# Kernel optimization log

Measured on AMD Instinct MI355X. Metric: run time of the kernel, lower is better.

## Reference

```python
import jax, jax.numpy as jnp
import numpy as np

B, N, C, H = 8, 1024, 1024, 16
HD = C // H
SCALE = HD ** -0.5

def setup_inputs() -> dict:
    key = jax.random.key(0)
    k1, k2, k3, k4 = jax.random.split(key, 4)
    x = jax.random.normal(k1, (B, N, C), dtype=jnp.float32)
    # torch nn.Linear weights: [out, in]
    w_qkv = jax.random.normal(k2, (3 * C, C), dtype=jnp.float32) * (C ** -0.5)
    w_proj = jax.random.normal(k3, (C, C), dtype=jnp.float32) * (C ** -0.5)
    b_proj = jax.random.normal(k4, (C,), dtype=jnp.float32) * 0.02
    return {"x": x, "w_qkv": w_qkv, "w_proj": w_proj, "b_proj": b_proj}

def reference(x, w_qkv, w_proj, b_proj):
    Bv, Nv, Cv = x.shape
    # qkv projection (no bias); torch Linear: x @ W^T
    qkv = jnp.einsum('bnc,dc->bnd', x, w_qkv)
    qkv = qkv.reshape(Bv, Nv, 3, H, HD).transpose(2, 0, 3, 1, 4)  # [3,B,H,N,hd]
    q, k, v = qkv[0], qkv[1], qkv[2]
    attn = jnp.einsum('bhnd,bhmd->bhnm', q, k) * SCALE  # [B,H,N,N]
    attn = jax.nn.softmax(attn, axis=-1)
    out = jnp.einsum('bhnm,bhmd->bhnd', attn, v)
    out = out.transpose(0, 2, 1, 3).reshape(Bv, Nv, Cv)
    out = jnp.einsum('bnc,dc->bnd', out, w_proj) + b_proj
    return out
```

## Files before the change

### kernel.cpp

```cpp
#include <hip/hip_runtime.h>


typedef __attribute__((ext_vector_type(8))) short bf16x8;
typedef __attribute__((ext_vector_type(4))) short bf16x4;
typedef __attribute__((ext_vector_type(4))) float f32x4;

__device__ __forceinline__ short f2bf(float f) {
    union { float f; unsigned u; } x;
    x.f = f;
    unsigned r = x.u + 0x7fffu + ((x.u >> 16) & 1u);
    return (short)(r >> 16);
}

__device__ __forceinline__ void load_lds16(const void* g, void* l) {
    __builtin_amdgcn_global_load_lds((const __attribute__((address_space(1))) unsigned*)g,
                                     (__attribute__((address_space(3))) unsigned*)l,
                                     16, 0, 0);
}

__global__ __launch_bounds__(256) void convert_all(const float* __restrict__ x,
                                                   const float* __restrict__ wqkv,
                                                   const float* __restrict__ wproj,
                                                   short* __restrict__ xb,
                                                   short* __restrict__ wqkvb,
                                                   short* __restrict__ wprojb) {
    int i = blockIdx.x * 256 + threadIdx.x;
    const float* src;
    short* dst;
    int j;
    if (i < 2097152)      { src = x;     dst = xb;     j = i; }
    else if (i < 2883584) { src = wqkv;  dst = wqkvb;  j = i - 2097152; }
    else                  { src = wproj; dst = wprojb; j = i - 2883584; }
    float4 v = *(const float4*)(src + j * 4);
    unsigned lo = (unsigned short)f2bf(v.x) | ((unsigned)(unsigned short)f2bf(v.y) << 16);
    unsigned hi = (unsigned short)f2bf(v.z) | ((unsigned)(unsigned short)f2bf(v.w) << 16);
    uint2 p; p.x = lo; p.y = hi;
    *(uint2*)(dst + j * 4) = p;
}

template<int EPI, int NTX>
__global__ __launch_bounds__(256, 3) void gemm97(const short* __restrict__ A,
                                                 const short* __restrict__ Bt,
                                                 short* __restrict__ q,
                                                 short* __restrict__ kk,
                                                 short* __restrict__ vt,
                                                 const float* __restrict__ bias,
                                                 float* __restrict__ out) {
    __shared__ alignas(16) short As[128][64];
    __shared__ alignas(16) short Bs[128][64];
    const int K = 1024;
    constexpr int NWG = 64 * NTX;
    constexpr int CHUNK = NWG / 8;

    const int bid = blockIdx.x;
    const int tile = (bid & 7) * CHUNK + (bid >> 3);
    const int m0 = (tile / NTX) * 128;
    const int n0 = (tile % NTX) * 128;

    const int t = threadIdx.x;
    const int w = t >> 6, lane = t & 63, quad = lane >> 4, l16 = lane & 15;
    const int wm = (w >> 1) * 64, wn = (w & 1) * 64;
    const int sw = l16 & 7;

    const int srow = t >> 3;
    const int scol = ((t & 7) ^ (srow & 7)) * 8;
    const short* Ag = A  + (m0 + srow) * K + scol;
    const short* Bg = Bt + (n0 + srow) * K + scol;
    short* const Asw = &As[w * 8][0];
    short* const Bsw = &Bs[w * 8][0];

    f32x4 acc[4][4];
    #pragma unroll
    for (int mi = 0; mi < 4; ++mi)
        #pragma unroll
        for (int ni = 0; ni < 4; ++ni) acc[mi][ni] = (f32x4){0.f, 0.f, 0.f, 0.f};

    #pragma unroll 1
    for (int kt = 0; kt < 16; ++kt) {
        __syncthreads();
        #pragma unroll
        for (int r = 0; r < 4; ++r)
            load_lds16(Ag + r * 32 * K + kt * 64, Asw + r * 32 * 64);
        #pragma unroll
        for (int r = 0; r < 4; ++r)
            load_lds16(Bg + r * 32 * K + kt * 64, Bsw + r * 32 * 64);
        __syncthreads();

        bf16x8 af[4][2], bf[4][2];
        #pragma unroll
        for (int mi = 0; mi < 4; ++mi)
            #pragma unroll
            for (int c = 0; c < 2; ++c)
                af[mi][c] = *(const bf16x8*)&As[wm + mi * 16 + l16][((quad + 4 * c) ^ sw) * 8];
        #pragma unroll
        for (int ni = 0; ni < 4; ++ni)
            #pragma unroll
            for (int c = 0; c < 2; ++c)
                bf[ni][c] = *(const bf16x8*)&Bs[wn + ni * 16 + l16][((quad + 4 * c) ^ sw) * 8];
        #pragma unroll
        for (int mi = 0; mi < 4; ++mi)
            #pragma unroll
            for (int ni = 0; ni < 4; ++ni) {
                acc[mi][ni] = __builtin_amdgcn_mfma_f32_16x16x32_bf16(af[mi][0], bf[ni][0], acc[mi][ni], 0, 0, 0);
                acc[mi][ni] = __builtin_amdgcn_mfma_f32_16x16x32_bf16(af[mi][1], bf[ni][1], acc[mi][ni], 0, 0, 0);
            }
    }

    if (EPI == 0) {
        const float QS = 0.125f * 1.44269504088896f;
        #pragma unroll
        for (int ni = 0; ni < 4; ++ni) {
            int col = n0 + wn + ni * 16 + l16;
            int sect = col >> 10;
            int c = col & 1023;
            int h = c >> 6, dd = c & 63;
            #pragma unroll
            for (int mi = 0; mi < 4; ++mi) {
                #pragma unroll
                for (int r = 0; r < 4; ++r) {
                    int m = m0 + wm + mi * 16 + quad * 4 + r;
                    int b = m >> 10, i = m & 1023;
                    float v = acc[mi][ni][r];
                    if (sect == 0)      q[((b * 16 + h) * 1024 + i) * 64 + dd] = f2bf(v * QS);
                    else if (sect == 1) kk[((b * 16 + h) * 1024 + i) * 64 + dd] = f2bf(v);
                    else                vt[((b * 16 + h) * 64 + dd) * 1024 + i] = f2bf(v);
                }
            }
        }
    } else {
        #pragma unroll
        for (int ni = 0; ni < 4; ++ni) {
            int col = n0 + wn + ni * 16 + l16;
            float bv = bias[col];
            #pragma unroll
            for (int mi = 0; mi < 4; ++mi) {
                #pragma unroll
                for (int r = 0; r < 4; ++r) {
                    int m = m0 + wm + mi * 16 + quad * 4 + r;
                    out[m * 1024 + col] = acc[mi][ni][r] + bv;
                }
            }
        }
    }
}

__global__ __launch_bounds__(256) void attn_kernel(const short* __restrict__ q,
                                                   const short* __restrict__ k,
                                                   const short* __restrict__ vt,
                                                   short* __restrict__ ao) {
    __shared__ alignas(16) short Ks[2][64][72];
    __shared__ alignas(16) short Vs[2][64][72];

    const int bh = blockIdx.y, qt = blockIdx.x;
    const int t = threadIdx.x, w = t >> 6, lane = t & 63, quad = lane >> 4, l16 = lane & 15;
    const short* qg = q  + (bh * 1024 + qt * 128) * 64;
    const short* kg = k  + bh * 65536;
    const short* vg = vt + bh * 65536;

    bf16x8 qf[2][2];
    for (int mi = 0; mi < 2; ++mi) {
        const short* qr = qg + (w * 32 + mi * 16 + l16) * 64;
        qf[mi][0] = *(const bf16x8*)(qr + quad * 8);
        qf[mi][1] = *(const bf16x8*)(qr + 32 + quad * 8);
    }

    const int r0 = t >> 3,          c80 = (t & 7) * 8;
    const int r1 = (t + 256) >> 3,  c81 = c80;

    float rs[2] = {0.f, 0.f};
    f32x4 oaccT[2][4];
    for (int mi = 0; mi < 2; ++mi)
        for (int dt = 0; dt < 4; ++dt) oaccT[mi][dt] = (f32x4){0.f, 0.f, 0.f, 0.f};

    {
        float4 a = *(const float4*)&kg[r0 * 64 + c80];
        float4 b = *(const float4*)&kg[r1 * 64 + c81];
        float4 c = *(const float4*)&vg[r0 * 1024 + c80];
        float4 d = *(const float4*)&vg[r1 * 1024 + c81];
        *(float4*)&Ks[0][r0][c80] = a;  *(float4*)&Ks[0][r1][c81] = b;
        *(float4*)&Vs[0][r0][c80] = c;  *(float4*)&Vs[0][r1][c81] = d;
    }

    for (int jt = 0; jt < 16; ++jt) {
        const int cur = jt & 1;
        asm volatile("s_waitcnt lgkmcnt(0)" ::: "memory");
        asm volatile("s_barrier" ::: "memory");

        float4 kr0, kr1, vr0, vr1;
        if (jt < 15) {
            int jn = jt + 1;
            kr0 = *(const float4*)&kg[(jn * 64 + r0) * 64 + c80];
            kr1 = *(const float4*)&kg[(jn * 64 + r1) * 64 + c81];
            vr0 = *(const float4*)&vg[r0 * 1024 + jn * 64 + c80];
            vr1 = *(const float4*)&vg[r1 * 1024 + jn * 64 + c81];
        }

        for (int js = 0; js < 4; ++js) {
            bf16x8 kf0 = *(const bf16x8*)&Ks[cur][js * 16 + l16][quad * 8];
            bf16x8 kf1 = *(const bf16x8*)&Ks[cur][js * 16 + l16][32 + quad * 8];
            bf16x4 vtf[4];
            for (int dt = 0; dt < 4; ++dt)
                vtf[dt] = *(const bf16x4*)&Vs[cur][dt * 16 + l16][js * 16 + quad * 4];
            for (int mi = 0; mi < 2; ++mi) {
                f32x4 s = (f32x4){0.f, 0.f, 0.f, 0.f};
                s = __builtin_amdgcn_mfma_f32_16x16x32_bf16(kf0, qf[mi][0], s, 0, 0, 0);
                s = __builtin_amdgcn_mfma_f32_16x16x32_bf16(kf1, qf[mi][1], s, 0, 0, 0);
                bf16x4 pfrag;
                for (int r = 0; r < 4; ++r) {
                    float p = __builtin_amdgcn_exp2f(s[r]);
                    rs[mi] += p;
                    pfrag[r] = f2bf(p);
                }
                for (int dt = 0; dt < 4; ++dt)
                    oaccT[mi][dt] = __builtin_amdgcn_mfma_f32_16x16x16bf16_1k(
                        vtf[dt], pfrag, oaccT[mi][dt], 0, 0, 0);
            }
        }

        if (jt < 15) {
            const int nxt = cur ^ 1;
            *(float4*)&Ks[nxt][r0][c80] = kr0;  *(float4*)&Ks[nxt][r1][c81] = kr1;
            *(float4*)&Vs[nxt][r0][c80] = vr0;  *(float4*)&Vs[nxt][r1][c81] = vr1;
        }
    }

    for (int mi = 0; mi < 2; ++mi) {
        rs[mi] += __shfl_xor(rs[mi], 16, 64);
        rs[mi] += __shfl_xor(rs[mi], 32, 64);
    }

    const int b = bh >> 4, h = bh & 15;
    for (int mi = 0; mi < 2; ++mi) {
        float inv = 1.0f / rs[mi];
        int i = qt * 128 + w * 32 + mi * 16 + l16;
        short* aor = ao + (b * 1024 + i) * 1024 + h * 64;
        for (int dt = 0; dt < 4; ++dt) {
            bf16x4 o4;
            for (int r = 0; r < 4; ++r) o4[r] = f2bf(oaccT[mi][dt][r] * inv);
            *(bf16x4*)(aor + dt * 16 + quad * 4) = o4;
        }
    }
}

extern "C" void kernel_launch(void* const* d_in, const int* in_sizes, int n_in,
                              void* d_out, int out_size, void* d_ws, size_t ws_size,
                              hipStream_t stream) {
    const float* x      = (const float*)d_in[0];
    const float* w_qkv  = (const float*)d_in[1];
    const float* w_proj = (const float*)d_in[2];
    const float* b_proj = (const float*)d_in[3];
    float* out = (float*)d_out;

    char* ws = (char*)d_ws;
    short* xb     = (short*)(ws);
    short* wqkvb  = (short*)(ws + 16777216);
    short* wprojb = (short*)(ws + 23068672);
    short* qb     = (short*)(ws + 25165824);
    short* kb     = (short*)(ws + 41943040);
    short* vtb    = (short*)(ws + 58720256);
    short* aob    = (short*)(ws + 75497472);

    convert_all<<<12288, 256, 0, stream>>>(x, w_qkv, w_proj, xb, wqkvb, wprojb);
    gemm97<0, 24><<<1536, 256, 0, stream>>>(xb, wqkvb, qb, kb, vtb, nullptr, nullptr);
    attn_kernel<<<dim3(8, 128), 256, 0, stream>>>(qb, kb, vtb, aob);
    gemm97<1, 8><<<512, 256, 0, stream>>>(aob, wprojb, nullptr, nullptr, nullptr, b_proj, out);
}
```

Measured before the change: 240.0 us.

## Rewrite GEMMs with 256x256 tiles, 8 waves, and double-buffered async LDS staging

Replaces the 128x128 single-buffered GEMM with a 256x256 tile kernel using 512 threads and 128KB of dynamic LDS. The next K-tile is prefetched into the other buffer while the current one is consumed, with vmcnt and barrier waits placed by hand and s_setprio raised around MFMA bursts. The goal is to hide global-load latency and improve data reuse per loaded byte. The cost is fewer workgroups: 384 and 128 blocks on a GPU with 256 CUs, which may cause wave-quantization losses, especially in the projection GEMM. It also brings higher register pressure and hand-tuned waitcnt counts that are easy to get wrong.

```diff
diff --git a/kernel.cpp b/kernel.cpp
--- a/kernel.cpp
+++ b/kernel.cpp
@@ -39,72 +39,120 @@
 }
 
 template<int EPI, int NTX>
-__global__ __launch_bounds__(256, 3) void gemm97(const short* __restrict__ A,
+__global__ __launch_bounds__(512, 2) void gemmkp(const short* __restrict__ A,
                                                  const short* __restrict__ Bt,
                                                  short* __restrict__ q,
                                                  short* __restrict__ kk,
                                                  short* __restrict__ vt,
                                                  const float* __restrict__ bias,
                                                  float* __restrict__ out) {
-    __shared__ alignas(16) short As[128][64];
-    __shared__ alignas(16) short Bs[128][64];
+    extern __shared__ short lds[];
+    short* const As = lds;
+    short* const Bs = lds + 32768;
     const int K = 1024;
-    constexpr int NWG = 64 * NTX;
+    constexpr int NWG = 32 * NTX;
     constexpr int CHUNK = NWG / 8;
 
     const int bid = blockIdx.x;
     const int tile = (bid & 7) * CHUNK + (bid >> 3);
-    const int m0 = (tile / NTX) * 128;
-    const int n0 = (tile % NTX) * 128;
+    const int m0 = (tile / NTX) * 256;
+    const int n0 = (tile % NTX) * 256;
 
     const int t = threadIdx.x;
     const int w = t >> 6, lane = t & 63, quad = lane >> 4, l16 = lane & 15;
-    const int wm = (w >> 1) * 64, wn = (w & 1) * 64;
-    const int sw = l16 & 7;
-
-    const int srow = t >> 3;
-    const int scol = ((t & 7) ^ (srow & 7)) * 8;
-    const short* Ag = A  + (m0 + srow) * K + scol;
-    const short* Bg = Bt + (n0 + srow) * K + scol;
-    short* const Asw = &As[w * 8][0];
-    short* const Bsw = &Bs[w * 8][0];
-
-    f32x4 acc[4][4];
+    const int wm = (w >> 2) * 128, wn = (w & 3) * 64;
+    const int swA = l16 & 7, swB = (l16 >> 1) & 3;
+
+    const int srA = t >> 3;
+    const int scA = ((t & 7) ^ (srA & 7)) * 8;
+    const int srB = t >> 2;
+    const int scB = ((t & 3) ^ ((srB >> 1) & 3)) * 8;
+
+    const short* Ag = A  + (m0 + srA) * K + scA;
+    const short* Bg = Bt + (n0 + srB) * K + scB;
+
+    f32x4 acc[8][4];
     #pragma unroll
-    for (int mi = 0; mi < 4; ++mi)
+    for (int mi = 0; mi < 8; ++mi)
         #pragma unroll
         for (int ni = 0; ni < 4; ++ni) acc[mi][ni] = (f32x4){0.f, 0.f, 0.f, 0.f};
 
+    bf16x8 af[4], bf[4];
+
+#define STG_A(kt_, h_) do { \
+    load_lds16(Ag + ((h_) * 64) * 1024 + (kt_) * 64, \
+               As + ((kt_) & 1) * 16384 + ((h_) * 64 + w * 8) * 64); \
+    load_lds16(Ag + ((h_) * 64 + 128) * 1024 + (kt_) * 64, \
+               As + ((kt_) & 1) * 16384 + ((h_) * 64 + 128 + w * 8) * 64); } while (0)
+#define STG_B(kt_, kap_) do { \
+    load_lds16(Bg + (kt_) * 64 + (kap_) * 32, \
+               Bs + ((kt_) & 1) * 16384 + (kap_) * 8192 + (w * 16) * 32); \
+    load_lds16(Bg + 128 * 1024 + (kt_) * 64 + (kap_) * 32, \
+               Bs + ((kt_) & 1) * 16384 + (kap_) * 8192 + (128 + w * 16) * 32); } while (0)
+
+#define READ_FRAGS(h_, kap_) do { \
+    _Pragma("unroll") \
+    for (int mi = 0; mi < 4; ++mi) \
+        af[mi] = *(const bf16x8*)(Ar + (wm + (h_) * 64 + mi * 16 + l16) * 64 + (((kap_) * 4 + quad) ^ swA) * 8); \
+    _Pragma("unroll") \
+    for (int ni = 0; ni < 4; ++ni) \
+        bf[ni] = *(const bf16x8*)(Br + (kap_) * 8192 + (wn + ni * 16 + l16) * 32 + (quad ^ swB) * 8); } while (0)
+
+#define MFMA16(h_) do { \
+    __builtin_amdgcn_s_setprio(1); \
+    _Pragma("unroll") \
+    for (int mi = 0; mi < 4; ++mi) \
+        _Pragma("unroll") \
+        for (int ni = 0; ni < 4; ++ni) \
+            acc[(h_) * 4 + mi][ni] = __builtin_amdgcn_mfma_f32_16x16x32_bf16(af[mi], bf[ni], acc[(h_) * 4 + mi][ni], 0, 0, 0); \
+    __builtin_amdgcn_s_setprio(0); } while (0)
+
+#define BAR   asm volatile("s_barrier" ::: "memory")
+#define LGKM0 asm volatile("s_waitcnt lgkmcnt(0)" ::: "memory")
+#define VM(n) asm volatile("s_waitcnt vmcnt(" #n ")" ::: "memory")
+
+    STG_A(0, 0); STG_B(0, 0); STG_A(0, 1); STG_B(0, 1);
+    STG_A(1, 0); STG_B(1, 0);
+    VM(8);
+    BAR;
+
     #pragma unroll 1
     for (int kt = 0; kt < 16; ++kt) {
-        __syncthreads();
-        #pragma unroll
-        for (int r = 0; r < 4; ++r)
-            load_lds16(Ag + r * 32 * K + kt * 64, Asw + r * 32 * 64);
-        #pragma unroll
-        for (int r = 0; r < 4; ++r)
-            load_lds16(Bg + r * 32 * K + kt * 64, Bsw + r * 32 * 64);
-        __syncthreads();
-
-        bf16x8 af[4][2], bf[4][2];
-        #pragma unroll
-        for (int mi = 0; mi < 4; ++mi)
-            #pragma unroll
-            for (int c = 0; c < 2; ++c)
-                af[mi][c] = *(const bf16x8*)&As[wm + mi * 16 + l16][((quad + 4 * c) ^ sw) * 8];
-        #pragma unroll
-        for (int ni = 0; ni < 4; ++ni)
-            #pragma unroll
-            for (int c = 0; c < 2; ++c)
-                bf[ni][c] = *(const bf16x8*)&Bs[wn + ni * 16 + l16][((quad + 4 * c) ^ sw) * 8];
-        #pragma unroll
-        for (int mi = 0; mi < 4; ++mi)
-            #pragma unroll
-            for (int ni = 0; ni < 4; ++ni) {
-                acc[mi][ni] = __builtin_amdgcn_mfma_f32_16x16x32_bf16(af[mi][0], bf[ni][0], acc[mi][ni], 0, 0, 0);
-                acc[mi][ni] = __builtin_amdgcn_mfma_f32_16x16x32_bf16(af[mi][1], bf[ni][1], acc[mi][ni], 0, 0, 0);
-            }
-    }
+        const short* Ar = As + (kt & 1) * 16384;
+        const short* Br = Bs + (kt & 1) * 16384;
+
+        READ_FRAGS(0, 0);
+        if (kt < 15) { STG_A(kt + 1, 1); STG_B(kt + 1, 1); }
+        BAR; LGKM0;
+        MFMA16(0);
+        if (kt < 15) VM(8); else VM(0);
+        BAR;
+
+        READ_FRAGS(0, 1);
+        BAR; LGKM0;
+        MFMA16(0);
+        BAR;
+
+        READ_FRAGS(1, 0);
+        if (kt < 14) STG_A(kt + 2, 0);
+        BAR; LGKM0;
+        MFMA16(1);
+        BAR;
+
+        READ_FRAGS(1, 1);
+        if (kt < 14) STG_B(kt + 2, 0);
+        BAR; LGKM0;
+        MFMA16(1);
+        if (kt < 14) VM(8); else if (kt == 14) VM(4);
+        BAR;
+    }
+#undef STG_A
+#undef STG_B
+#undef READ_FRAGS
+#undef MFMA16
+#undef BAR
+#undef LGKM0
+#undef VM
 
     if (EPI == 0) {
         const float QS = 0.125f * 1.44269504088896f;
@@ -115,7 +163,7 @@
             int c = col & 1023;
             int h = c >> 6, dd = c & 63;
             #pragma unroll
-            for (int mi = 0; mi < 4; ++mi) {
+            for (int mi = 0; mi < 8; ++mi) {
                 #pragma unroll
                 for (int r = 0; r < 4; ++r) {
                     int m = m0 + wm + mi * 16 + quad * 4 + r;
@@ -133,7 +181,7 @@
             int col = n0 + wn + ni * 16 + l16;
             float bv = bias[col];
             #pragma unroll
-            for (int mi = 0; mi < 4; ++mi) {
+            for (int mi = 0; mi < 8; ++mi) {
                 #pragma unroll
                 for (int r = 0; r < 4; ++r) {
                     int m = m0 + wm + mi * 16 + quad * 4 + r;
@@ -260,8 +308,17 @@
     short* vtb    = (short*)(ws + 58720256);
     short* aob    = (short*)(ws + 75497472);
 
+    static bool s_init = false;
+    if (!s_init) {
+        hipFuncSetAttribute(reinterpret_cast<const void*>(&gemmkp<0, 12>),
+                            hipFuncAttributeMaxDynamicSharedMemorySize, 131072);
+        hipFuncSetAttribute(reinterpret_cast<const void*>(&gemmkp<1, 4>),
+                            hipFuncAttributeMaxDynamicSharedMemorySize, 131072);
+        s_init = true;
+    }
+
     convert_all<<<12288, 256, 0, stream>>>(x, w_qkv, w_proj, xb, wqkvb, wprojb);
-    gemm97<0, 24><<<1536, 256, 0, stream>>>(xb, wqkvb, qb, kb, vtb, nullptr, nullptr);
+    gemmkp<0, 12><<<384, 512, 131072, stream>>>(xb, wqkvb, qb, kb, vtb, nullptr, nullptr);
     attn_kernel<<<dim3(8, 128), 256, 0, stream>>>(qb, kb, vtb, aob);
-    gemm97<1, 8><<<512, 256, 0, stream>>>(aob, wprojb, nullptr, nullptr, nullptr, b_proj, out);
-}
+    gemmkp<1, 4><<<128, 512, 131072, stream>>>(aob, wprojb, nullptr, nullptr, nullptr, b_proj, out);
+}
```

New measurement: 280.7 us. 17.0% more time.

## Double-buffer LDS tiles in GEMM kernels to overlap global loads with MFMA

Applied to the files above, without the earlier changes.

Converts both GEMM kernels to a two-stage LDS pipeline using 64KB of dynamic shared memory, prefetching the next K tile while the current one feeds the MFMAs. This removes one of the two barriers per iteration and is meant to hide global-to-LDS load latency. In exchange, LDS use doubles and the launch bound drops from 3 to 2 workgroups per CU, which lowers occupancy.

```diff
diff --git a/kernel.cpp b/kernel.cpp
--- a/kernel.cpp
+++ b/kernel.cpp
@@ -39,15 +39,14 @@
 }
 
 template<int EPI, int NTX>
-__global__ __launch_bounds__(256, 3) void gemm97(const short* __restrict__ A,
+__global__ __launch_bounds__(256, 2) void gemmdb(const short* __restrict__ A,
                                                  const short* __restrict__ Bt,
                                                  short* __restrict__ q,
                                                  short* __restrict__ kk,
                                                  short* __restrict__ vt,
                                                  const float* __restrict__ bias,
                                                  float* __restrict__ out) {
-    __shared__ alignas(16) short As[128][64];
-    __shared__ alignas(16) short Bs[128][64];
+    extern __shared__ short lds[];
     const int K = 1024;
     constexpr int NWG = 64 * NTX;
     constexpr int CHUNK = NWG / 8;
@@ -66,8 +65,7 @@
     const int scol = ((t & 7) ^ (srow & 7)) * 8;
     const short* Ag = A  + (m0 + srow) * K + scol;
     const short* Bg = Bt + (n0 + srow) * K + scol;
-    short* const Asw = &As[w * 8][0];
-    short* const Bsw = &Bs[w * 8][0];
+    const int w8 = w * 8 * 64;
 
     f32x4 acc[4][4];
     #pragma unroll
@@ -75,28 +73,35 @@
         #pragma unroll
         for (int ni = 0; ni < 4; ++ni) acc[mi][ni] = (f32x4){0.f, 0.f, 0.f, 0.f};
 
+#define STG(kt_, d_) do { \
+    _Pragma("unroll") \
+    for (int r = 0; r < 4; ++r) \
+        load_lds16(Ag + r * 32 * K + (kt_) * 64, lds + (d_) * 8192 + r * 32 * 64 + w8); \
+    _Pragma("unroll") \
+    for (int r = 0; r < 4; ++r) \
+        load_lds16(Bg + r * 32 * K + (kt_) * 64, lds + 16384 + (d_) * 8192 + r * 32 * 64 + w8); } while (0)
+
+    STG(0, 0);
+    __syncthreads();
+
     #pragma unroll 1
     for (int kt = 0; kt < 16; ++kt) {
-        __syncthreads();
-        #pragma unroll
-        for (int r = 0; r < 4; ++r)
-            load_lds16(Ag + r * 32 * K + kt * 64, Asw + r * 32 * 64);
-        #pragma unroll
-        for (int r = 0; r < 4; ++r)
-            load_lds16(Bg + r * 32 * K + kt * 64, Bsw + r * 32 * 64);
-        __syncthreads();
-
+        const int d = kt & 1;
+        if (kt < 15) STG(kt + 1, d ^ 1);
+
+        const short* Ar = lds + d * 8192;
+        const short* Br = lds + 16384 + d * 8192;
         bf16x8 af[4][2], bf[4][2];
         #pragma unroll
         for (int mi = 0; mi < 4; ++mi)
             #pragma unroll
             for (int c = 0; c < 2; ++c)
-                af[mi][c] = *(const bf16x8*)&As[wm + mi * 16 + l16][((quad + 4 * c) ^ sw) * 8];
+                af[mi][c] = *(const bf16x8*)(Ar + (wm + mi * 16 + l16) * 64 + (((quad + 4 * c) ^ sw) * 8));
         #pragma unroll
         for (int ni = 0; ni < 4; ++ni)
             #pragma unroll
             for (int c = 0; c < 2; ++c)
-                bf[ni][c] = *(const bf16x8*)&Bs[wn + ni * 16 + l16][((quad + 4 * c) ^ sw) * 8];
+                bf[ni][c] = *(const bf16x8*)(Br + (wn + ni * 16 + l16) * 64 + (((quad + 4 * c) ^ sw) * 8));
         #pragma unroll
         for (int mi = 0; mi < 4; ++mi)
             #pragma unroll
@@ -104,7 +109,9 @@
                 acc[mi][ni] = __builtin_amdgcn_mfma_f32_16x16x32_bf16(af[mi][0], bf[ni][0], acc[mi][ni], 0, 0, 0);
                 acc[mi][ni] = __builtin_amdgcn_mfma_f32_16x16x32_bf16(af[mi][1], bf[ni][1], acc[mi][ni], 0, 0, 0);
             }
-    }
+        if (kt < 15) __syncthreads();
+    }
+#undef STG
 
     if (EPI == 0) {
         const float QS = 0.125f * 1.44269504088896f;
@@ -260,8 +267,17 @@
     short* vtb    = (short*)(ws + 58720256);
     short* aob    = (short*)(ws + 75497472);
 
+    static bool s_init = false;
+    if (!s_init) {
+        hipFuncSetAttribute(reinterpret_cast<const void*>(&gemmdb<0, 24>),
+                            hipFuncAttributeMaxDynamicSharedMemorySize, 65536);
+        hipFuncSetAttribute(reinterpret_cast<const void*>(&gemmdb<1, 8>),
+                            hipFuncAttributeMaxDynamicSharedMemorySize, 65536);
+        s_init = true;
+    }
+
     convert_all<<<12288, 256, 0, stream>>>(x, w_qkv, w_proj, xb, wqkvb, wprojb);
-    gemm97<0, 24><<<1536, 256, 0, stream>>>(xb, wqkvb, qb, kb, vtb, nullptr, nullptr);
+    gemmdb<0, 24><<<1536, 256, 65536, stream>>>(xb, wqkvb, qb, kb, vtb, nullptr, nullptr);
     attn_kernel<<<dim3(8, 128), 256, 0, stream>>>(qb, kb, vtb, aob);
-    gemm97<1, 8><<<512, 256, 0, stream>>>(aob, wprojb, nullptr, nullptr, nullptr, b_proj, out);
-}
+    gemmdb<1, 8><<<512, 256, 65536, stream>>>(aob, wprojb, nullptr, nullptr, nullptr, b_proj, out);
+}
```

New measurement: 254.2 us. +5.9%, slower.

## Double-buffer QKV GEMM in dynamic LDS with 8 waves per block

Applied to the files above, without the earlier changes.

Splits the templated GEMM into a dedicated QKV kernel and a projection kernel. The QKV kernel now uses 512 threads (8 waves, each computing a 64x32 sub-tile) and double-buffered LDS staging through global_load_lds, so the next K-tile loads while the current one is multiplied. That takes one barrier per iteration and is meant to hide global memory latency. In exchange it uses 64KB of dynamic LDS, which can limit occupancy, and each wave does less MFMA work per LDS fragment read.

```diff
diff --git a/kernel.cpp b/kernel.cpp
--- a/kernel.cpp
+++ b/kernel.cpp
@@ -38,17 +38,109 @@
     *(uint2*)(dst + j * 4) = p;
 }
 
-template<int EPI, int NTX>
-__global__ __launch_bounds__(256, 3) void gemm97(const short* __restrict__ A,
-                                                 const short* __restrict__ Bt,
-                                                 short* __restrict__ q,
-                                                 short* __restrict__ kk,
-                                                 short* __restrict__ vt,
-                                                 const float* __restrict__ bias,
-                                                 float* __restrict__ out) {
+__global__ __launch_bounds__(512, 4) void gemm_qkv5(const short* __restrict__ A,
+                                                    const short* __restrict__ Bt,
+                                                    short* __restrict__ q,
+                                                    short* __restrict__ kk,
+                                                    short* __restrict__ vt) {
+    extern __shared__ short lds[];
+    const int K = 1024;
+    constexpr int NTX = 24;
+    constexpr int NWG = 64 * NTX;
+    constexpr int CHUNK = NWG / 8;
+
+    const int bid = blockIdx.x;
+    const int tile = (bid & 7) * CHUNK + (bid >> 3);
+    const int m0 = (tile / NTX) * 128;
+    const int n0 = (tile % NTX) * 128;
+
+    const int t = threadIdx.x;
+    const int w = t >> 6, lane = t & 63, quad = lane >> 4, l16 = lane & 15;
+    const int wm = (w >> 2) * 64, wn = (w & 3) * 32;
+    const int sw = l16 & 7;
+
+    const int srow = t >> 3;
+    const int scol = ((t & 7) ^ (srow & 7)) * 8;
+    const short* Ag = A  + (m0 + srow) * K + scol;
+    const short* Bg = Bt + (n0 + srow) * K + scol;
+    const int w8 = w * 8 * 64;
+
+    f32x4 acc[4][2];
+    #pragma unroll
+    for (int mi = 0; mi < 4; ++mi)
+        #pragma unroll
+        for (int ni = 0; ni < 2; ++ni) acc[mi][ni] = (f32x4){0.f, 0.f, 0.f, 0.f};
+
+#define STG(kt_, d_) do { \
+    _Pragma("unroll") \
+    for (int r = 0; r < 2; ++r) \
+        load_lds16(Ag + r * 64 * K + (kt_) * 64, lds + (d_) * 8192 + r * 64 * 64 + w8); \
+    _Pragma("unroll") \
+    for (int r = 0; r < 2; ++r) \
+        load_lds16(Bg + r * 64 * K + (kt_) * 64, lds + 16384 + (d_) * 8192 + r * 64 * 64 + w8); } while (0)
+
+    STG(0, 0);
+    __syncthreads();
+
+    #pragma unroll 1
+    for (int kt = 0; kt < 16; ++kt) {
+        const int d = kt & 1;
+        if (kt < 15) STG(kt + 1, d ^ 1);
+
+        const short* Ar = lds + d * 8192;
+        const short* Br = lds + 16384 + d * 8192;
+        bf16x8 af[4][2], bf[2][2];
+        #pragma unroll
+        for (int mi = 0; mi < 4; ++mi)
+            #pragma unroll
+            for (int c = 0; c < 2; ++c)
+                af[mi][c] = *(const bf16x8*)(Ar + (wm + mi * 16 + l16) * 64 + (((quad + 4 * c) ^ sw) * 8));
+        #pragma unroll
+        for (int ni = 0; ni < 2; ++ni)
+            #pragma unroll
+            for (int c = 0; c < 2; ++c)
+                bf[ni][c] = *(const bf16x8*)(Br + (wn + ni * 16 + l16) * 64 + (((quad + 4 * c) ^ sw) * 8));
+        #pragma unroll
+        for (int mi = 0; mi < 4; ++mi)
+            #pragma unroll
+            for (int ni = 0; ni < 2; ++ni) {
+                acc[mi][ni] = __builtin_amdgcn_mfma_f32_16x16x32_bf16(af[mi][0], bf[ni][0], acc[mi][ni], 0, 0, 0);
+                acc[mi][ni] = __builtin_amdgcn_mfma_f32_16x16x32_bf16(af[mi][1], bf[ni][1], acc[mi][ni], 0, 0, 0);
+            }
+        if (kt < 15) __syncthreads();
+    }
+#undef STG
+
+    const float QS = 0.125f * 1.44269504088896f;
+    #pragma unroll
+    for (int ni = 0; ni < 2; ++ni) {
+        int col = n0 + wn + ni * 16 + l16;
+        int sect = col >> 10;
+        int c = col & 1023;
+        int h = c >> 6, dd = c & 63;
+        #pragma unroll
+        for (int mi = 0; mi < 4; ++mi) {
+            #pragma unroll
+            for (int r = 0; r < 4; ++r) {
+                int m = m0 + wm + mi * 16 + quad * 4 + r;
+                int b = m >> 10, i = m & 1023;
+                float v = acc[mi][ni][r];
+                if (sect == 0)      q[((b * 16 + h) * 1024 + i) * 64 + dd] = f2bf(v * QS);
+                else if (sect == 1) kk[((b * 16 + h) * 1024 + i) * 64 + dd] = f2bf(v);
+                else                vt[((b * 16 + h) * 64 + dd) * 1024 + i] = f2bf(v);
+            }
+        }
+    }
+}
+
+__global__ __launch_bounds__(256, 3) void gemm_proj9(const short* __restrict__ A,
+                                                     const short* __restrict__ Bt,
+                                                     const float* __restrict__ bias,
+                                                     float* __restrict__ out) {
     __shared__ alignas(16) short As[128][64];
     __shared__ alignas(16) short Bs[128][64];
     const int K = 1024;
+    constexpr int NTX = 8;
     constexpr int NWG = 64 * NTX;
     constexpr int CHUNK = NWG / 8;
 
@@ -106,39 +198,16 @@
             }
     }
 
-    if (EPI == 0) {
-        const float QS = 0.125f * 1.44269504088896f;
-        #pragma unroll
-        for (int ni = 0; ni < 4; ++ni) {
-            int col = n0 + wn + ni * 16 + l16;
-            int sect = col >> 10;
-            int c = col & 1023;
-            int h = c >> 6, dd = c & 63;
-            #pragma unroll
-            for (int mi = 0; mi < 4; ++mi) {
-                #pragma unroll
-                for (int r = 0; r < 4; ++r) {
-                    int m = m0 + wm + mi * 16 + quad * 4 + r;
-                    int b = m >> 10, i = m & 1023;
-                    float v = acc[mi][ni][r];
-                    if (sect == 0)      q[((b * 16 + h) * 1024 + i) * 64 + dd] = f2bf(v * QS);
-                    else if (sect == 1) kk[((b * 16 + h) * 1024 + i) * 64 + dd] = f2bf(v);
-                    else                vt[((b * 16 + h) * 64 + dd) * 1024 + i] = f2bf(v);
-                }
-            }
-        }
-    } else {
-        #pragma unroll
-        for (int ni = 0; ni < 4; ++ni) {
-            int col = n0 + wn + ni * 16 + l16;
-            float bv = bias[col];
-            #pragma unroll
-            for (int mi = 0; mi < 4; ++mi) {
-                #pragma unroll
-                for (int r = 0; r < 4; ++r) {
-                    int m = m0 + wm + mi * 16 + quad * 4 + r;
-                    out[m * 1024 + col] = acc[mi][ni][r] + bv;
-                }
+    #pragma unroll
+    for (int ni = 0; ni < 4; ++ni) {
+        int col = n0 + wn + ni * 16 + l16;
+        float bv = bias[col];
+        #pragma unroll
+        for (int mi = 0; mi < 4; ++mi) {
+            #pragma unroll
+            for (int r = 0; r < 4; ++r) {
+                int m = m0 + wm + mi * 16 + quad * 4 + r;
+                out[m * 1024 + col] = acc[mi][ni][r] + bv;
             }
         }
     }
@@ -260,8 +329,15 @@
     short* vtb    = (short*)(ws + 58720256);
     short* aob    = (short*)(ws + 75497472);
 
+    static bool s_init = false;
+    if (!s_init) {
+        hipFuncSetAttribute(reinterpret_cast<const void*>(&gemm_qkv5),
+                            hipFuncAttributeMaxDynamicSharedMemorySize, 65536);
+        s_init = true;
+    }
+
     convert_all<<<12288, 256, 0, stream>>>(x, w_qkv, w_proj, xb, wqkvb, wprojb);
-    gemm97<0, 24><<<1536, 256, 0, stream>>>(xb, wqkvb, qb, kb, vtb, nullptr, nullptr);
+    gemm_qkv5<<<1536, 512, 65536, stream>>>(xb, wqkvb, qb, kb, vtb);
     attn_kernel<<<dim3(8, 128), 256, 0, stream>>>(qb, kb, vtb, aob);
-    gemm97<1, 8><<<512, 256, 0, stream>>>(aob, wprojb, nullptr, nullptr, nullptr, b_proj, out);
-}
+    gemm_proj9<<<512, 256, 0, stream>>>(aob, wprojb, b_proj, out);
+}
```

Result: slower. 261.2 us (+8.8%).
